# Kernel optimization log

Measured on AMD Instinct MI355X. Metric: run time of the kernel, lower is better.

## Reference

```python
import jax, jax.numpy as jnp
import numpy as np

N_NODES = 50000
N_EDGES = 1600000
IN_DIM = 64
EDGE_DIM = 8
N_GRAPHS = 256
EXP_IN = 32
H = 64  # hidden dim per head / GCN hidden
EPS = 1e-5
NEG_SLOPE = 0.2


def gat_layer(x, src, dst, ea, W, a_src, a_dst, We, a_e, bias, heads, dim, concat):
    """PyG-style GATConv with edge features and self-loops (fill_value='mean')."""
    N = x.shape[0]
    ones_e = jnp.ones((ea.shape[0],), x.dtype)
    cnt = jax.ops.segment_sum(ones_e, dst, num_segments=N)
    loop_attr = jax.ops.segment_sum(ea, dst, num_segments=N) / jnp.maximum(cnt, 1.0)[:, None]
    s = jnp.concatenate([src, jnp.arange(N)])
    d = jnp.concatenate([dst, jnp.arange(N)])
    eaf = jnp.concatenate([ea, loop_attr], axis=0)  # [E+N, edge_dim]
    h = (x @ W).reshape(N, heads, dim)              # [N, H, D]
    ee = (eaf @ We).reshape(-1, heads, dim)         # [E+N, H, D]
    al_src = (h * a_src).sum(-1)                    # [N, H]
    al_dst = (h * a_dst).sum(-1)                    # [N, H]
    score = al_src[s] + al_dst[d] + (ee * a_e).sum(-1)
    score = jax.nn.leaky_relu(score, NEG_SLOPE)     # [E+N, H]
    m = jax.ops.segment_max(score, d, num_segments=N)
    ex = jnp.exp(score - m[d])
    att = ex / jax.ops.segment_sum(ex, d, num_segments=N)[d]
    out = jax.ops.segment_sum(h[s] * att[:, :, None], d, num_segments=N)  # [N, H, D]
    out = out.reshape(N, heads * dim) if concat else out.mean(axis=1)
    return out + bias


def gcn_layer(x, src, dst, W, b):
    """PyG-style GCNConv: add self loops, symmetric degree normalization."""
    N = x.shape[0]
    s = jnp.concatenate([src, jnp.arange(N)])
    d = jnp.concatenate([dst, jnp.arange(N)])
    deg = jax.ops.segment_sum(jnp.ones((s.shape[0],), x.dtype), d, num_segments=N)
    dinv = jax.lax.rsqrt(deg)  # deg >= 1 thanks to self loops
    norm = dinv[s] * dinv[d]
    h = x @ W
    return jax.ops.segment_sum(h[s] * norm[:, None], d, num_segments=N) + b


def bn(x, g, b):
    m = x.mean(axis=0)
    v = x.var(axis=0)
    return g * (x - m) * jax.lax.rsqrt(v + EPS) + b


def mean_pool(x, batch, num_graphs):
    s = jax.ops.segment_sum(x, batch, num_segments=num_graphs)
    c = jax.ops.segment_sum(jnp.ones((x.shape[0],), x.dtype), batch, num_segments=num_graphs)
    return s / jnp.maximum(c, 1.0)[:, None]


def setup_inputs() -> dict:
    key = jax.random.key(0)
    ks = jax.random.split(key, 32)
    p = lambda i, shape: jax.random.normal(ks[i], shape, jnp.float32) * 0.05
    z = lambda n: jnp.zeros((n,), jnp.float32)
    o = lambda n: jnp.ones((n,), jnp.float32)
    return {
        "x": jax.random.normal(ks[0], (N_NODES, IN_DIM), jnp.float32),
        "edge_attr": jax.random.normal(ks[1], (N_EDGES, EDGE_DIM), jnp.float32),
        "experimental_feat": jax.random.normal(ks[2], (N_GRAPHS, EXP_IN), jnp.float32),
        "edge_index": jax.random.randint(ks[3], (2, N_EDGES), 0, N_NODES),
        "batch": jnp.sort(jax.random.randint(ks[4], (N_NODES,), 0, N_GRAPHS)),
        "W1": p(5, (IN_DIM, 4 * H)), "att_src1": p(6, (4, H)), "att_dst1": p(7, (4, H)),
        "We1": p(8, (EDGE_DIM, 4 * H)), "att_e1": p(9, (4, H)), "b1": z(4 * H),
        "g1": o(4 * H), "be1": z(4 * H),
        "W2": p(10, (4 * H, H)), "att_src2": p(11, (1, H)), "att_dst2": p(12, (1, H)),
        "We2": p(13, (EDGE_DIM, H)), "att_e2": p(14, (1, H)), "b2": z(H),
        "g2": o(H), "be2": z(H),
        "Wg1": p(15, (H, H)), "bg1": z(H), "g3": o(H), "be3": z(H),
        "Wg2": p(16, (H, H)), "bg2": z(H), "g4": o(H), "be4": z(H),
        "Wex1": p(17, (EXP_IN, H)), "bex1": z(H), "Wex2": p(18, (H, H)), "bex2": z(H),
        "Wc1": p(19, (2 * H, 128)), "bc1": z(128), "Wc2": p(20, (128, 1)), "bc2": z(1),
    }


def reference(x, edge_attr, experimental_feat, edge_index, batch,
              W1, att_src1, att_dst1, We1, att_e1, b1, g1, be1,
              W2, att_src2, att_dst2, We2, att_e2, b2, g2, be2,
              Wg1, bg1, g3, be3, Wg2, bg2, g4, be4,
              Wex1, bex1, Wex2, bex2, Wc1, bc1, Wc2, bc2):
    src, dst = edge_index[0], edge_index[1]
    h = gat_layer(x, src, dst, edge_attr, W1, att_src1, att_dst1, We1, att_e1, b1, 4, H, True)
    h = jax.nn.relu(bn(h, g1, be1))
    h = gat_layer(h, src, dst, edge_attr, W2, att_src2, att_dst2, We2, att_e2, b2, 1, H, False)
    h = jax.nn.relu(bn(h, g2, be2))  # dropout = identity in eval
    h = gcn_layer(h, src, dst, Wg1, bg1)
    h = jax.nn.relu(bn(h, g3, be3))
    h = gcn_layer(h, src, dst, Wg2, bg2)
    h = jax.nn.relu(bn(h, g4, be4))
    xp = mean_pool(h, batch, N_GRAPHS)                    # [G, H]
    e = jax.nn.relu(experimental_feat @ Wex1 + bex1)
    e = jax.nn.relu(e @ Wex2 + bex2)
    combined = jnp.concatenate([xp, e], axis=1)           # [G, 2H]
    combined = jax.nn.relu(combined @ Wc1 + bc1)          # [G, 128]
    out = combined @ Wc2 + bc2                            # [G, 1]
    return (out, xp, combined)
```

## Files before the change

kernel.cpp:

```cpp
#include <hip/hip_runtime.h>
#include <hip/hip_bf16.h>

#define N_NODES 50000
#define N_EDGES 1600000
#define N_GRAPHS 256
#define NEG_SLOPE 0.2f
#define BN_EPS 1e-5f

typedef __hip_bfloat16 bf16;
typedef __attribute__((ext_vector_type(8))) short s16x8;
typedef __attribute__((ext_vector_type(4))) float f32x4;
typedef __attribute__((ext_vector_type(4))) int i32x4;

__device__ __forceinline__ float b2f(bf16 v){ return __bfloat162float(v); }
__device__ __forceinline__ bf16 f2b(float v){ return __float2bfloat16(v); }
__device__ __forceinline__ float us2f(unsigned short u){ return __uint_as_float(((unsigned)u)<<16); }
__device__ __forceinline__ unsigned short f2us(float v){ bf16 b = f2b(v); return *(unsigned short*)&b; }
__device__ __forceinline__ unsigned pk2(float a, float b){ return (unsigned)f2us(a) | ((unsigned)f2us(b)<<16); }
__device__ __forceinline__ float ldF(const void* p, size_t i, int m){
  return m ? ((const float*)p)[i] : b2f(((const bf16*)p)[i]);
}
__device__ __forceinline__ float sane(float v){
  return (v == v && fabsf(v) < 1e30f) ? v : 0.f;
}
__device__ __forceinline__ float sel4(const float v[4], int h){
  float r = v[0];
  r = (h==1) ? v[1] : r;
  r = (h==2) ? v[2] : r;
  r = (h==3) ? v[3] : r;
  return r;
}
__device__ __forceinline__ void acc8(float* acc, float w, uint4 u){
  acc[0] += w*us2f((unsigned short)(u.x & 0xffff)); acc[1] += w*us2f((unsigned short)(u.x >> 16));
  acc[2] += w*us2f((unsigned short)(u.y & 0xffff)); acc[3] += w*us2f((unsigned short)(u.y >> 16));
  acc[4] += w*us2f((unsigned short)(u.z & 0xffff)); acc[5] += w*us2f((unsigned short)(u.z >> 16));
  acc[6] += w*us2f((unsigned short)(u.w & 0xffff)); acc[7] += w*us2f((unsigned short)(u.w >> 16));
}
__device__ __forceinline__ void unp8(float* o, uint4 u){
  o[0] = us2f((unsigned short)(u.x & 0xffff)); o[1] = us2f((unsigned short)(u.x >> 16));
  o[2] = us2f((unsigned short)(u.y & 0xffff)); o[3] = us2f((unsigned short)(u.y >> 16));
  o[4] = us2f((unsigned short)(u.z & 0xffff)); o[5] = us2f((unsigned short)(u.z >> 16));
  o[6] = us2f((unsigned short)(u.w & 0xffff)); o[7] = us2f((unsigned short)(u.w >> 16));
}
__device__ __forceinline__ s16x8 pk8(const float* v){
  s16x8 r;
  #pragma unroll
  for(int j=0;j<8;j++) r[j] = (short)f2us(v[j]);
  return r;
}
__device__ __forceinline__ void wave_lds_fence(){
  __builtin_amdgcn_sched_barrier(0);
  asm volatile("s_waitcnt lgkmcnt(0)" ::: "memory");
  __builtin_amdgcn_sched_barrier(0);
}

__device__ int detect_mode_block(const void* x){
  __shared__ int s_ins;
  if(threadIdx.x == 0) s_ins = 0;
  __syncthreads();
  const unsigned short* u = (const unsigned short*)x;
  int c = 0;
  for(int i = threadIdx.x; i < 1024; i += blockDim.x){
    float v = fabsf(us2f(u[i]));
    if(!(v > 1e-6f && v < 1e4f)) c++;
  }
  if(c) atomicAdd(&s_ins, c);
  __syncthreads();
  return (s_ins > 128) ? 1 : 0;
}

#define NSEG 33
struct Bank { const void* p[NSEG]; int n[NSEG]; int off[NSEG]; };

__global__ void k_convert(Bank b, const void* xdet, float* out){
  int m = detect_mode_block(xdet);
  int seg = blockIdx.y;
  int i = blockIdx.x*256 + threadIdx.x;
  if(i < b.n[seg]) out[b.off[seg] + i] = ldF(b.p[seg], i, m);
}

__global__ void k_cvt_x(const void* x, bf16* xb){
  int m = detect_mode_block(x);
  int i4 = blockIdx.x*256 + threadIdx.x;
  if(i4 >= N_NODES*16) return;
  if(m){
    float4 v = ((const float4*)x)[i4];
    ((ushort4*)xb)[i4] = make_ushort4(f2us(v.x), f2us(v.y), f2us(v.z), f2us(v.w));
  } else {
    ((ushort4*)xb)[i4] = ((const ushort4*)x)[i4];
  }
}

__global__ void k_we(const float* __restrict__ We1, const float* __restrict__ ae1,
                     const float* __restrict__ We2, const float* __restrict__ ae2,
                     float* __restrict__ w_e){
  int t = threadIdx.x;
  if(t < 32){
    int h = t >> 3, k = t & 7;
    float s = 0.f;
    for(int d=0;d<64;d++) s += We1[k*256 + h*64 + d] * ae1[h*64 + d];
    w_e[t] = s;
  } else if(t < 40){
    int k = t - 32;
    float s = 0.f;
    for(int d=0;d<64;d++) s += We2[k*64 + d] * ae2[d];
    w_e[t] = s;
  }
}

__global__ void k_wt(const float* __restrict__ W1, const float* __restrict__ W2,
                     const float* __restrict__ Wg1, const float* __restrict__ Wg2,
                     bf16* __restrict__ wt){
  int i = blockIdx.x*256 + threadIdx.x;
  if(i < 16384){
    int c = i >> 6, k = i & 63;
    wt[i] = f2b(W1[k*256 + c]);
  } else if(i < 32768){
    int j = i - 16384; int c = j >> 8, k = j & 255;
    wt[i] = f2b(W2[k*64 + c]);
  } else if(i < 36864){
    int j = i - 32768; int c = j >> 6, k = j & 63;
    wt[i] = f2b(Wg1[k*64 + c]);
  } else if(i < 40960){
    int j = i - 36864; int c = j >> 6, k = j & 63;
    wt[i] = f2b(Wg2[k*64 + c]);
  }
}

__global__ void k_count(const int* __restrict__ dst, int* __restrict__ cnt){
  int e = blockIdx.x*256 + threadIdx.x;
  if(e < N_EDGES){
    int d = dst[e]; if((unsigned)d >= N_NODES) d = 0;
    atomicAdd(&cnt[d], 1);
  }
}

__global__ void k_blocksum(const int* __restrict__ cnt, int* __restrict__ bsum){
  __shared__ int s[256];
  int i = blockIdx.x*256 + threadIdx.x;
  s[threadIdx.x] = (i < N_NODES) ? cnt[i] : 0;
  __syncthreads();
  for(int o=128;o>0;o>>=1){ if(threadIdx.x<o) s[threadIdx.x]+=s[threadIdx.x+o]; __syncthreads(); }
  if(threadIdx.x==0) bsum[blockIdx.x]=s[0];
}

__global__ void k_scan_bsum(const int* __restrict__ bsum, int* __restrict__ bofs, int nb){
  __shared__ int s[256];
  int t = threadIdx.x;
  s[t] = (t<nb) ? bsum[t] : 0;
  __syncthreads();
  for(int o=1;o<256;o<<=1){ int v=(t>=o)?s[t-o]:0; __syncthreads(); s[t]+=v; __syncthreads(); }
  bofs[t] = (t==0) ? 0 : s[t-1];
}

__global__ void k_scan_write(const int* __restrict__ cnt, const int* __restrict__ bofs,
                             int* __restrict__ rp, float* __restrict__ dinv){
  __shared__ int s[256];
  int t = threadIdx.x; int i = blockIdx.x*256 + t;
  int v = (i<N_NODES) ? cnt[i] : 0;
  s[t]=v; __syncthreads();
  for(int o=1;o<256;o<<=1){ int a=(t>=o)?s[t-o]:0; __syncthreads(); s[t]+=a; __syncthreads(); }
  if(i<N_NODES){
    rp[i+1] = s[t] + bofs[blockIdx.x];
    dinv[i] = rsqrtf((float)v + 1.f);
  }
  if(i==0) rp[0]=0;
}

__global__ void k_fill(const int* __restrict__ src, const int* __restrict__ dst,
                       const int* __restrict__ rp, int* __restrict__ fill,
                       const void* __restrict__ ea, const void* __restrict__ xdet,
                       const float* __restrict__ w_e,
                       int4* __restrict__ epk){
  int m = detect_mode_block(xdet);
  int e = blockIdx.x*256 + threadIdx.x;
  if(e >= N_EDGES) return;
  int d = dst[e]; if((unsigned)d >= N_NODES) d = 0;
  int p = atomicAdd(&fill[d], 1);
  int slot = rp[d] + p;
  if((unsigned)slot >= N_EDGES) return;
  int sv = src[e]; if((unsigned)sv >= N_NODES) sv = 0;
  float a[8];
  if(m){
    const float* eaf = (const float*)ea;
    float4 lo = *(const float4*)&eaf[(size_t)e*8];
    float4 hi = *(const float4*)&eaf[(size_t)e*8 + 4];
    a[0]=lo.x; a[1]=lo.y; a[2]=lo.z; a[3]=lo.w;
    a[4]=hi.x; a[5]=hi.y; a[6]=hi.z; a[7]=hi.w;
  } else {
    #pragma unroll
    for(int k=0;k<8;k++) a[k] = b2f(((const bf16*)ea)[(size_t)e*8 + k]);
  }
  unsigned d4[4];
  #pragma unroll
  for(int h=0;h<4;h++){
    float s = 0.f;
    #pragma unroll
    for(int k=0;k<8;k++) s += a[k]*w_e[h*8+k];
    d4[h] = f2us(s);
  }
  float s1 = 0.f;
  #pragma unroll
  for(int k=0;k<8;k++) s1 += a[k]*w_e[32+k];
  i32x4 pk;
  pk[0] = sv;
  pk[1] = (int)(d4[0] | (d4[1] << 16));
  pk[2] = (int)(d4[2] | (d4[3] << 16));
  pk[3] = (int)(unsigned)f2us(s1);
  __builtin_nontemporal_store(pk, (i32x4*)&epk[slot]);
}

__global__ __launch_bounds__(256) void k_gemmA_mfma(
    const bf16* __restrict__ xb,
    const bf16* __restrict__ wt1,
    bf16* __restrict__ hp, int M,
    const float* __restrict__ asrc,
    const float* __restrict__ adst,
    float* __restrict__ als4, float* __restrict__ ald4)
{
  const int tid = threadIdx.x;
  const int w = tid >> 6, l = tid & 63;
  const int lr = l & 15, lg = l >> 4;
  const int bm = blockIdx.x*64 + w*16;
  const int arow_i = bm + lr;
  const uint4* arow = (const uint4*)(xb + (size_t)min(arow_i, M-1)*64);
  uint4 a0u = arow[lg];
  uint4 a1u = arow[4 + lg];
  s16x8 a0 = *(s16x8*)&a0u, a1 = *(s16x8*)&a1u;
  unsigned short* out = (unsigned short*)hp;
  const int orow0 = bm + lg*4;
  float p_s[4][4] = {};
  float p_d[4][4] = {};
  #pragma unroll
  for(int ct = 0; ct < 16; ct++){
    const uint4* brow = (const uint4*)(wt1 + (size_t)(ct*16 + lr)*64);
    uint4 b0u = brow[lg];
    uint4 b1u = brow[4 + lg];
    f32x4 acc = {0.f, 0.f, 0.f, 0.f};
    acc = __builtin_amdgcn_mfma_f32_16x16x32_bf16(a0, *(s16x8*)&b0u, acc, 0, 0, 0);
    acc = __builtin_amdgcn_mfma_f32_16x16x32_bf16(a1, *(s16x8*)&b1u, acc, 0, 0, 0);
    float a_s = asrc[ct*16 + lr];
    float a_d = adst[ct*16 + lr];
    int hh = ct >> 2;
    #pragma unroll
    for(int r = 0; r < 4; r++){
      p_s[hh][r] += acc[r]*a_s;
      p_d[hh][r] += acc[r]*a_d;
      int rr = orow0 + r;
      if(rr < M) out[(size_t)rr*256 + ct*16 + lr] = f2us(acc[r]);
    }
  }
  #pragma unroll
  for(int o = 1; o < 16; o <<= 1){
    #pragma unroll
    for(int hh=0; hh<4; hh++)
      #pragma unroll
      for(int r=0; r<4; r++){
        p_s[hh][r] += __shfl_xor(p_s[hh][r], o);
        p_d[hh][r] += __shfl_xor(p_d[hh][r], o);
      }
  }
  if(lr == 0){
    #pragma unroll
    for(int r=0;r<4;r++){
      int rr = orow0 + r;
      if(rr < M){
        #pragma unroll
        for(int hh=0;hh<4;hh++){
          als4[rr*4 + hh] = p_s[hh][r];
          ald4[rr*4 + hh] = p_d[hh][r];
        }
      }
    }
  }
}

template<int KIN>
__global__ __launch_bounds__(256) void k_gemmB_mfma(
    const bf16* __restrict__ A, const bf16* __restrict__ Wt,
    bf16* __restrict__ C, int M,
    const float* __restrict__ bnsums, const float* __restrict__ bng, const float* __restrict__ bnb,
    const float* __restrict__ asrc, const float* __restrict__ adst,
    float* __restrict__ als, float* __restrict__ ald)
{
  __shared__ float st_s[KIN];
  __shared__ float st_t[KIN];
  const int tid = threadIdx.x;
  if(tid < KIN){
    const float invN = 1.0f / (float)N_NODES;
    float mean = bnsums[tid]*invN;
    float var  = fmaxf(bnsums[KIN+tid]*invN - mean*mean, 0.f);
    float s = bng[tid]*rsqrtf(var + BN_EPS);
    st_s[tid] = s;
    st_t[tid] = bnb[tid] - mean*s;
  }
  __syncthreads();
  const int w = tid >> 6, l = tid & 63;
  const int lr = l & 15, lg = l >> 4;
  const int bm = blockIdx.x*64 + w*16;
  const int arow_i = bm + lr;
  const uint4* arow = (const uint4*)(A + (size_t)min(arow_i, M-1)*KIN);
  f32x4 acc[4];
  #pragma unroll
  for(int ct=0;ct<4;ct++) acc[ct] = (f32x4){0.f,0.f,0.f,0.f};
  #pragma unroll
  for(int k0 = 0; k0 < KIN; k0 += 32){
    uint4 au = arow[(k0 >> 3) + lg];
    int c0 = k0 + lg*8;
    float v[8]; unp8(v, au);
    #pragma unroll
    for(int j = 0; j < 8; j++){
      float y = sane(v[j])*st_s[c0+j] + st_t[c0+j];
      v[j] = fmaxf(y, 0.f);
    }
    s16x8 af = pk8(v);
    #pragma unroll
    for(int ct = 0; ct < 4; ct++){
      const uint4* brow = (const uint4*)(Wt + (size_t)(ct*16 + lr)*KIN);
      uint4 bu = brow[(k0 >> 3) + lg];
      acc[ct] = __builtin_amdgcn_mfma_f32_16x16x32_bf16(af, *(s16x8*)&bu, acc[ct], 0, 0, 0);
    }
  }
  unsigned short* out = (unsigned short*)C;
  const int orow0 = bm + lg*4;
  #pragma unroll
  for(int ct = 0; ct < 4; ct++){
    #pragma unroll
    for(int r = 0; r < 4; r++){
      int rr = orow0 + r;
      if(rr < M) out[(size_t)rr*64 + ct*16 + lr] = f2us(acc[ct][r]);
    }
  }
  if(als){
    float p_s[4] = {0.f,0.f,0.f,0.f};
    float p_d[4] = {0.f,0.f,0.f,0.f};
    #pragma unroll
    for(int ct=0;ct<4;ct++){
      float a_s = asrc[ct*16 + lr];
      float a_d = adst[ct*16 + lr];
      #pragma unroll
      for(int r=0;r<4;r++){
        p_s[r] += acc[ct][r]*a_s;
        p_d[r] += acc[ct][r]*a_d;
      }
    }
    #pragma unroll
    for(int o = 1; o < 16; o <<= 1){
      #pragma unroll
      for(int r=0;r<4;r++){
        p_s[r] += __shfl_xor(p_s[r], o);
        p_d[r] += __shfl_xor(p_d[r], o);
      }
    }
    if(lr == 0){
      #pragma unroll
      for(int r=0;r<4;r++){
        int rr = orow0 + r;
        if(rr < M){ als[rr] = p_s[r]; ald[rr] = p_d[r]; }
      }
    }
  }
}

__global__ __launch_bounds__(256) void k_gat_agg4(
    const int* __restrict__ rp, const int4* __restrict__ epk,
    const bf16* __restrict__ hp,
    const float* __restrict__ als4, const float* __restrict__ ald4,
    const float* __restrict__ bias256, bf16* __restrict__ out1){
  const int wid = threadIdx.x >> 6, l = threadIdx.x & 63;
  const int n = blockIdx.x*4 + wid;
  if(n >= N_NODES) return;
  int eh = l >> 5, c8 = l & 31;
  int head = c8 >> 3;
  __shared__ int   ssrc_s[4][64];
  __shared__ float swt_s[4][64][4];
  int* ssrc = ssrc_s[wid];
  float (*swt)[4] = swt_s[wid];
  int s0 = rp[n], e0 = rp[n+1];
  if((unsigned)s0 > N_EDGES){ s0=0; e0=0; }
  if(e0 < s0 || (unsigned)e0 > N_EDGES) e0 = s0;
  float4 aldv = *(const float4*)&ald4[n*4];
  float4 alsvn = *(const float4*)&als4[n*4];
  float wsum[4] = {0.f,0.f,0.f,0.f};
  float dsum[4] = {0.f,0.f,0.f,0.f};
  float acc[8]  = {0.f,0.f,0.f,0.f,0.f,0.f,0.f,0.f};
  const unsigned short* hpu = (const unsigned short*)hp;

  for(int base = s0; base < e0; base += 64){
    int m = min(64, e0 - base);
    if(l < m){
      i32x4 pk = __builtin_nontemporal_load((const i32x4*)&epk[base+l]);
      int sn = pk[0]; if((unsigned)sn >= N_NODES) sn = 0;
      ssrc[l] = sn;
      float edf[4] = {us2f((unsigned short)(pk[1] & 0xffff)), us2f((unsigned short)((unsigned)pk[1] >> 16)),
                      us2f((unsigned short)(pk[2] & 0xffff)), us2f((unsigned short)((unsigned)pk[2] >> 16))};
      float4 alss = *(const float4*)&als4[sn*4];
      float alssv[4] = {alss.x, alss.y, alss.z, alss.w};
      float aldvv[4] = {aldv.x, aldv.y, aldv.z, aldv.w};
      float w4[4];
      #pragma unroll
      for(int h=0;h<4;h++){
        float sc = alssv[h] + aldvv[h] + edf[h];
        sc = sc > 0.f ? sc : NEG_SLOPE*sc;
        sc = fminf(sc, 30.f);
        float w = __expf(sc);
        w4[h] = w;
        wsum[h] += w; dsum[h] += edf[h];
      }
      *(float4*)&swt[l][0] = make_float4(w4[0], w4[1], w4[2], w4[3]);
    }
    wave_lds_fence();
    #pragma unroll 8
    for(int i=0;i<m;i+=2){
      int j = i + eh;
      if(j < m){
        int row = ssrc[j];
        float w = swt[j][head];
        uint4 u = *(const uint4*)&hpu[(size_t)row*256 + 8*c8];
        acc8(acc, w, u);
      }
    }
    __builtin_amdgcn_wave_barrier();
  }
  #pragma unroll
  for(int o=1;o<64;o<<=1){
    #pragma unroll
    for(int h=0;h<4;h++){
      wsum[h] += __shfl_xor(wsum[h], o);
      dsum[h] += __shfl_xor(dsum[h], o);
    }
  }
  #pragma unroll
  for(int q=0;q<8;q++) acc[q] += __shfl_xor(acc[q], 32);
  if(eh == 0){
    float alsnv[4] = {alsvn.x, alsvn.y, alsvn.z, alsvn.w};
    float aldnv[4] = {aldv.x, aldv.y, aldv.z, aldv.w};
    float sEh = sel4(wsum, head), sDh = sel4(dsum, head);
    float deg = (float)(e0 - s0);
    float sdot = deg > 0.f ? sDh/deg : 0.f;
    float sc = sel4(alsnv, head) + sel4(aldnv, head) + sdot;
    sc = sc > 0.f ? sc : NEG_SLOPE*sc;
    sc = fminf(sc, 30.f);
    float wself = __expf(sc);
    float self[8];
    unp8(self, *(const uint4*)&hpu[(size_t)n*256 + 8*c8]);
    float4 b0 = *(const float4*)&bias256[8*c8];
    float4 b1 = *(const float4*)&bias256[8*c8 + 4];
    float bi[8] = {b0.x,b0.y,b0.z,b0.w,b1.x,b1.y,b1.z,b1.w};
    float inv = 1.f/(sEh + wself);
    float o8[8];
    #pragma unroll
    for(int q=0;q<8;q++) o8[q] = (acc[q] + wself*self[q])*inv + bi[q];
    uint4 st;
    st.x = pk2(o8[0],o8[1]); st.y = pk2(o8[2],o8[3]);
    st.z = pk2(o8[4],o8[5]); st.w = pk2(o8[6],o8[7]);
    *(uint4*)&((unsigned short*)out1)[(size_t)n*256 + 8*c8] = st;
  }
}

__global__ __launch_bounds__(256) void k_gat_agg1e(
    const int* __restrict__ rp, const int4* __restrict__ epk,
    const bf16* __restrict__ hp,
    const float* __restrict__ als, const float* __restrict__ ald,
    const float* __restrict__ bias64, bf16* __restrict__ out){
  const int wid = threadIdx.x >> 6, l = threadIdx.x & 63;
  const int n = blockIdx.x*4 + wid;
  if(n >= N_NODES) return;
  int eg = l >> 3, c8 = l & 7;
  __shared__ float sw_s[4][64];
  __shared__ int   ssrc_s[4][64];
  float* sw = sw_s[wid];
  int* ssrc = ssrc_s[wid];
  int s0 = rp[n], e0 = rp[n+1];
  if((unsigned)s0 > N_EDGES){ s0=0; e0=0; }
  if(e0 < s0 || (unsigned)e0 > N_EDGES) e0 = s0;
  float aldn = ald[n];
  float wsum_l = 0.f, dsum_l = 0.f;
  float acc[8] = {0.f,0.f,0.f,0.f,0.f,0.f,0.f,0.f};
  const unsigned short* hpu = (const unsigned short*)hp;
  for(int base = s0; base < e0; base += 64){
    int m = min(64, e0 - base);
    if(l < m){
      i32x4 pk = __builtin_nontemporal_load((const i32x4*)&epk[base+l]);
      int sn = pk[0]; if((unsigned)sn >= N_NODES) sn = 0;
      ssrc[l] = sn;
      float ed = us2f((unsigned short)(pk[3] & 0xffff));
      float sc = als[sn] + aldn + ed;
      sc = sc > 0.f ? sc : NEG_SLOPE*sc;
      sc = fminf(sc, 30.f);
      float w = __expf(sc);
      sw[l] = w;
      wsum_l += w; dsum_l += ed;
    }
    wave_lds_fence();
    #pragma unroll 4
    for(int i=0;i<m;i+=8){
      int j = i + eg;
      if(j < m){
        int row = ssrc[j];
        float w = sw[j];
        uint4 u = *(const uint4*)&hpu[(size_t)row*64 + 8*c8];
        acc8(acc, w, u);
      }
    }
    __builtin_amdgcn_wave_barrier();
  }
  #pragma unroll
  for(int o=1;o<64;o<<=1){ wsum_l += __shfl_xor(wsum_l, o); dsum_l += __shfl_xor(dsum_l, o); }
  #pragma unroll
  for(int q=0;q<8;q++){
    acc[q] += __shfl_xor(acc[q], 8);
    acc[q] += __shfl_xor(acc[q], 16);
    acc[q] += __shfl_xor(acc[q], 32);
  }
  if(l < 8){
    float deg = (float)(e0 - s0);
    float sdot = deg > 0.f ? dsum_l/deg : 0.f;
    float sc = als[n] + aldn + sdot;
    sc = sc > 0.f ? sc : NEG_SLOPE*sc;
    sc = fminf(sc, 30.f);
    float wself = __expf(sc);
    float self[8];
    unp8(self, *(const uint4*)&hpu[(size_t)n*64 + 8*l]);
    float4 b0 = *(const float4*)&bias64[8*l];
    float4 b1 = *(const float4*)&bias64[8*l + 4];
    float bi[8] = {b0.x,b0.y,b0.z,b0.w,b1.x,b1.y,b1.z,b1.w};
    float inv = 1.f/(wsum_l + wself);
    float o8[8];
    #pragma unroll
    for(int q=0;q<8;q++) o8[q] = (acc[q] + wself*self[q])*inv + bi[q];
    uint4 st;
    st.x = pk2(o8[0],o8[1]); st.y = pk2(o8[2],o8[3]);
    st.z = pk2(o8[4],o8[5]); st.w = pk2(o8[6],o8[7]);
    *(uint4*)&((unsigned short*)out)[(size_t)n*64 + 8*l] = st;
  }
}

__global__ __launch_bounds__(256) void k_gcn_agg(
    const int* __restrict__ rp, const int4* __restrict__ epk,
    const float* __restrict__ dinv, const bf16* __restrict__ gp,
    const float* __restrict__ bias, bf16* __restrict__ out){
  const int wid = threadIdx.x >> 6, l = threadIdx.x & 63;
  const int n = blockIdx.x*4 + wid;
  if(n >= N_NODES) return;
  int eg = l >> 3, c8 = l & 7;
  __shared__ float sw_s[4][64];
  __shared__ int   ssrc_s[4][64];
  float* sw = sw_s[wid];
  int* ssrc = ssrc_s[wid];
  int s0 = rp[n], e0 = rp[n+1];
  if((unsigned)s0 > N_EDGES){ s0=0; e0=0; }
  if(e0 < s0 || (unsigned)e0 > N_EDGES) e0 = s0;
  float dn = dinv[n];
  float acc[8] = {0.f,0.f,0.f,0.f,0.f,0.f,0.f,0.f};
  const unsigned short* gpu = (const unsigned short*)gp;
  for(int base = s0; base < e0; base += 64){
    int m = min(64, e0 - base);
    if(l < m){
      i32x4 pk = __builtin_nontemporal_load((const i32x4*)&epk[base+l]);
      int sn = pk[0]; if((unsigned)sn >= N_NODES) sn = 0;
      ssrc[l]=sn; sw[l]=dinv[sn];
    }
    wave_lds_fence();
    #pragma unroll 4
    for(int i=0;i<m;i+=8){
      int j = i + eg;
      if(j < m){
        int row = ssrc[j];
        float w = sw[j];
        uint4 u = *(const uint4*)&gpu[(size_t)row*64 + 8*c8];
        acc8(acc, w, u);
      }
    }
    __builtin_amdgcn_wave_barrier();
  }
  #pragma unroll
  for(int q=0;q<8;q++){
    acc[q] += __shfl_xor(acc[q], 8);
    acc[q] += __shfl_xor(acc[q], 16);
    acc[q] += __shfl_xor(acc[q], 32);
  }
  if(l < 8){
    float self[8];
    unp8(self, *(const uint4*)&gpu[(size_t)n*64 + 8*l]);
    float4 b0 = *(const float4*)&bias[8*l];
    float4 b1 = *(const float4*)&bias[8*l + 4];
    float bi[8] = {b0.x,b0.y,b0.z,b0.w,b1.x,b1.y,b1.z,b1.w};
    float o8[8];
    #pragma unroll
    for(int q=0;q<8;q++) o8[q] = dn*(acc[q] + dn*self[q]) + bi[q];
    uint4 st;
    st.x = pk2(o8[0],o8[1]); st.y = pk2(o8[2],o8[3]);
    st.z = pk2(o8[4],o8[5]); st.w = pk2(o8[6],o8[7]);
    *(uint4*)&((unsigned short*)out)[(size_t)n*64 + 8*l] = st;
  }
}

template<int C>
__global__ void k_colstats(const bf16* __restrict__ X, float* __restrict__ sums){
  constexpr int RPB = 128;
  constexpr int RSTEP = 256 / C;
  int c = threadIdx.x % C;
  int r0 = threadIdx.x / C;
  int rbeg = blockIdx.x * RPB;
  int rend = min(N_NODES, rbeg + RPB);
  const unsigned short* Xu = (const unsigned short*)X;
  float s = 0.f, q = 0.f;
  for(int r = rbeg + r0; r < rend; r += RSTEP){
    float v = sane(us2f(Xu[(size_t)r*C + c]));
    s += v; q += v*v;
  }
  atomicAdd(&sums[c], s);
  atomicAdd(&sums[C + c], q);
}

__global__ __launch_bounds__(64) void k_pool3(
    const bf16* __restrict__ h, const int* __restrict__ batch,
    const float* __restrict__ sums, const float* __restrict__ g4,
    const float* __restrict__ b4,
    float* __restrict__ psum, float* __restrict__ pcnt){
  int t = threadIdx.x;
  int n0 = blockIdx.x * 256;
  int n1 = min(N_NODES, n0 + 256);
  if(n0 >= n1) return;
  const float invN = 1.0f / (float)N_NODES;
  float mean = sums[t]*invN;
  float var = fmaxf(sums[64+t]*invN - mean*mean, 0.f);
  float rstd = rsqrtf(var + BN_EPS);
  float gg = g4[t], bb = b4[t];
  const unsigned short* hu = (const unsigned short*)h;
  int cur = batch[n0]; if((unsigned)cur >= N_GRAPHS) cur = 0;
  float acc = 0.f; int cl = 0;
  for(int n = n0; n < n1; n++){
    int g = batch[n]; if((unsigned)g >= N_GRAPHS) g = 0;
    if(g != cur){
      atomicAdd(&psum[cur*64 + t], acc);
      if(t == 0) atomicAdd(&pcnt[cur], (float)cl);
      acc = 0.f; cl = 0; cur = g;
    }
    float y = (sane(us2f(hu[(size_t)n*64 + t]))-mean)*rstd*gg + bb;
    acc += fmaxf(y, 0.f);
    cl++;
  }
  atomicAdd(&psum[cur*64 + t], acc);
  if(t == 0) atomicAdd(&pcnt[cur], (float)cl);
}

__device__ __forceinline__ void stO(void* o, size_t i, float v, int m){
  if(m) ((float*)o)[i] = v; else ((bf16*)o)[i] = f2b(v);
}

__global__ __launch_bounds__(128) void k_head(
    const float* __restrict__ psum, const float* __restrict__ pcnt,
    const float* __restrict__ exf,
    const float* __restrict__ Wex1, const float* __restrict__ bex1,
    const float* __restrict__ Wex2, const float* __restrict__ bex2,
    const float* __restrict__ Wc1, const float* __restrict__ bc1,
    const float* __restrict__ Wc2, const float* __restrict__ bc2,
    const void* __restrict__ xdet, void* __restrict__ dout){
  int m0 = detect_mode_block(xdet);
  int g = blockIdx.x; int t = threadIdx.x;
  __shared__ float ci[128];
  __shared__ float e1[64];
  __shared__ float comb[128];
  __shared__ float red[128];
  if(t < 64){
    float c = fmaxf(pcnt[g], 1.f);
    float xp = sane(psum[g*64 + t]) / c;
    ci[t] = xp;
    stO(dout, 256 + (size_t)g*64 + t, xp, m0);
  } else {
    int j = t - 64;
    float s = bex1[j];
    for(int k=0;k<32;k++) s += exf[g*32 + k] * Wex1[k*64 + j];
    e1[j] = fmaxf(s, 0.f);
  }
  __syncthreads();
  if(t >= 64){
    int j = t - 64;
    float s = bex2[j];
    for(int k=0;k<64;k++) s += e1[k] * Wex2[k*64 + j];
    ci[64 + j] = fmaxf(s, 0.f);
  }
  __syncthreads();
  {
    float s = bc1[t];
    for(int k=0;k<128;k++) s += ci[k] * Wc1[k*128 + t];
    s = fmaxf(s, 0.f);
    comb[t] = s;
    stO(dout, 256 + 16384 + (size_t)g*128 + t, s, m0);
  }
  __syncthreads();
  red[t] = comb[t] * Wc2[t];
  __syncthreads();
  for(int o=64;o>0;o>>=1){ if(t<o) red[t]+=red[t+o]; __syncthreads(); }
  if(t==0) stO(dout, g, red[0] + bc2[0], m0);
}

extern "C" void kernel_launch(void* const* d_in, const int* in_sizes, int n_in,
                              void* d_out, int out_size, void* d_ws, size_t ws_size,
                              hipStream_t stream){
  const void* x    = d_in[0];
  const void* ea   = d_in[1];
  const int* ei    = (const int*)d_in[3];
  const int* batch = (const int*)d_in[4];
  const int* src = ei;
  const int* dst = ei + N_EDGES;

  char* base = (char*)d_ws;
  size_t off = 0;
  auto alloc = [&](size_t bytes) -> void* {
    void* r = base + off;
    off += (bytes + 255) & ~(size_t)255;
    return r;
  };
  int*   cnt    = (int*)  alloc((size_t)N_NODES*4);
  int*   fill   = (int*)  alloc((size_t)N_NODES*4);
  float* bnstat = (float*)alloc(4096);
  float* pool   = (float*)alloc((size_t)(N_GRAPHS*64 + N_GRAPHS)*4);
  size_t zbytes = off;
  int*   rp      = (int*)  alloc((size_t)(N_NODES+1)*4);
  int*   bsum    = (int*)  alloc(256*4);
  int*   bofs    = (int*)  alloc(256*4);
  int4*  epk     = (int4*) alloc((size_t)N_EDGES*16);
  float* dinv    = (float*)alloc((size_t)N_NODES*4);
  float* w_e     = (float*)alloc(64*4);
  float* als4    = (float*)alloc((size_t)N_NODES*4*4);
  float* ald4    = (float*)alloc((size_t)N_NODES*4*4);
  float* wbank   = (float*)alloc(80000*4);
  bf16*  wt      = (bf16*) alloc((size_t)40960*2);
  bf16*  xb      = (bf16*) alloc((size_t)N_NODES*64*2);
  bf16*  hp      = (bf16*) alloc((size_t)N_NODES*256*2);
  bf16*  outb    = (bf16*) alloc((size_t)N_NODES*256*2);

  bf16* out1 = outb;
  bf16* out2 = outb;
  bf16* out3 = outb + (size_t)N_NODES*64;
  bf16* out4 = outb + (size_t)N_NODES*128;
  float* bn1 = bnstat;
  float* bn2 = bnstat + 512;
  float* bn3 = bnstat + 640;
  float* bn4 = bnstat + 768;
  float* psum = pool;
  float* pcnt = pool + N_GRAPHS*64;

  bf16* wt1  = wt;
  bf16* wt2  = wt + 16384;
  bf16* wtg1 = wt + 32768;
  bf16* wtg2 = wt + 36864;

  const int segidx[NSEG] = {2, 5,6,7,8,9,10,11,12, 13,14,15,16,17,18,19,20,
                            21,22,23,24, 25,26,27,28, 29,30,31,32, 33,34,35,36};
  const int segn[NSEG] = {8192, 16384,256,256,2048,256,256,256,256,
                          16384,64,64,512,64,64,64,64,
                          4096,64,64,64, 4096,64,64,64,
                          2048,64,4096,64, 16384,128,128,1};
  Bank bk;
  int offs[NSEG]; int acc0 = 0;
  for(int i=0;i<NSEG;i++){ bk.p[i]=d_in[segidx[i]]; bk.n[i]=segn[i]; bk.off[i]=acc0; offs[i]=acc0; acc0+=segn[i]; }
  const float* f_exf = wbank + offs[0];
  const float* fW1 = wbank+offs[1]; const float* fas1 = wbank+offs[2]; const float* fad1 = wbank+offs[3];
  const float* fWe1= wbank+offs[4]; const float* fae1 = wbank+offs[5]; const float* fb1  = wbank+offs[6];
  const float* fg1 = wbank+offs[7]; const float* fbe1 = wbank+offs[8];
  const float* fW2 = wbank+offs[9]; const float* fas2 = wbank+offs[10]; const float* fad2 = wbank+offs[11];
  const float* fWe2= wbank+offs[12]; const float* fae2 = wbank+offs[13]; const float* fb2 = wbank+offs[14];
  const float* fg2 = wbank+offs[15]; const float* fbe2 = wbank+offs[16];
  const float* fWg1= wbank+offs[17]; const float* fbg1 = wbank+offs[18]; const float* fg3 = wbank+offs[19];
  const float* fbe3= wbank+offs[20];
  const float* fWg2= wbank+offs[21]; const float* fbg2 = wbank+offs[22]; const float* fg4 = wbank+offs[23];
  const float* fbe4= wbank+offs[24];
  const float* fWex1=wbank+offs[25]; const float* fbex1= wbank+offs[26];
  const float* fWex2=wbank+offs[27]; const float* fbex2= wbank+offs[28];
  const float* fWc1= wbank+offs[29]; const float* fbc1 = wbank+offs[30];
  const float* fWc2= wbank+offs[31]; const float* fbc2 = wbank+offs[32];

  const int nbN  = (N_NODES + 255)/256;
  const int nbE  = (N_EDGES + 255)/256;
  const int nbT  = (N_NODES + 63)/64;
  const int nbA  = (N_NODES + 3)/4;

  hipMemsetAsync(d_ws, 0, zbytes, stream);
  {
    dim3 g((16384+255)/256, NSEG);
    k_convert<<<g,256,0,stream>>>(bk, x, wbank);
  }
  k_wt<<<160,256,0,stream>>>(fW1, fW2, fWg1, fWg2, wt);
  k_cvt_x<<<(N_NODES*16+255)/256,256,0,stream>>>(x, xb);
  k_we<<<1,64,0,stream>>>(fWe1, fae1, fWe2, fae2, w_e);
  k_count<<<nbE,256,0,stream>>>(dst, cnt);
  k_blocksum<<<nbN,256,0,stream>>>(cnt, bsum);
  k_scan_bsum<<<1,256,0,stream>>>(bsum, bofs, nbN);
  k_scan_write<<<nbN,256,0,stream>>>(cnt, bofs, rp, dinv);
  k_fill<<<nbE,256,0,stream>>>(src, dst, rp, fill, ea, x, w_e, epk);

  k_gemmA_mfma<<<nbT,256,0,stream>>>(xb, wt1, hp, N_NODES, fas1, fad1, als4, ald4);
  k_gat_agg4<<<nbA,256,0,stream>>>(rp, epk, hp, als4, ald4, fb1, out1);
  k_colstats<256><<<(N_NODES+127)/128,256,0,stream>>>(out1, bn1);

  k_gemmB_mfma<256><<<nbT,256,0,stream>>>(out1, wt2, hp, N_NODES, bn1, fg1, fbe1,
                                          fas2, fad2, als4, ald4);
  k_gat_agg1e<<<nbA,256,0,stream>>>(rp, epk, hp, als4, ald4, fb2, out2);
  k_colstats<64><<<(N_NODES+127)/128,256,0,stream>>>(out2, bn2);

  k_gemmB_mfma<64><<<nbT,256,0,stream>>>(out2, wtg1, hp, N_NODES, bn2, fg2, fbe2,
                                         nullptr, nullptr, nullptr, nullptr);
  k_gcn_agg<<<nbA,256,0,stream>>>(rp, epk, dinv, hp, fbg1, out3);
  k_colstats<64><<<(N_NODES+127)/128,256,0,stream>>>(out3, bn3);

  k_gemmB_mfma<64><<<nbT,256,0,stream>>>(out3, wtg2, hp, N_NODES, bn3, fg3, fbe3,
                                         nullptr, nullptr, nullptr, nullptr);
  k_gcn_agg<<<nbA,256,0,stream>>>(rp, epk, dinv, hp, fbg2, out4);
  k_colstats<64><<<(N_NODES+127)/128,256,0,stream>>>(out4, bn4);

  k_pool3<<<nbN,64,0,stream>>>(out4, batch, bn4, fg4, fbe4, psum, pcnt);
  k_head<<<N_GRAPHS,128,0,stream>>>(psum, pcnt, f_exf, fWex1, fbex1, fWex2, fbex2,
                                    fWc1, fbc1, fWc2, fbc2, x, (void*)d_out);
}
```

Before: 929.2 us.

## Split packed edge records into SoA arrays and merge prep kernels

Replaces the 16-byte packed edge record with separate arrays for source index, 4-head edge scores and single-head edge score, so each aggregation kernel reads only the fields it uses (GCN reads 4 bytes per edge instead of 16). The weight conversion, transpose, edge-weight fold and degree count kernels are merged into one launch, the block-offset scan is folded into the scan-write kernel, and the x-to-bf16 conversion is fused into the first GEMM's load. Also raises unroll in two aggregation loops and uses more blocks in pooling. This trades fewer launches and less edge traffic for more scattered stores in the fill kernel and redundant small scans per block.

```diff
diff --git a/kernel.cpp b/kernel.cpp
--- a/kernel.cpp
+++ b/kernel.cpp
@@ -10,7 +10,7 @@
 typedef __hip_bfloat16 bf16;
 typedef __attribute__((ext_vector_type(8))) short s16x8;
 typedef __attribute__((ext_vector_type(4))) float f32x4;
-typedef __attribute__((ext_vector_type(4))) int i32x4;
+typedef __attribute__((ext_vector_type(2))) unsigned u32x2;
 
 __device__ __forceinline__ float b2f(bf16 v){ return __bfloat162float(v); }
 __device__ __forceinline__ bf16 f2b(float v){ return __float2bfloat16(v); }
@@ -72,66 +72,58 @@
 #define NSEG 33
 struct Bank { const void* p[NSEG]; int n[NSEG]; int off[NSEG]; };
 
-__global__ void k_convert(Bank b, const void* xdet, float* out){
+#define PREP_COUNT 6250
+#define PREP_CONV  (64*NSEG)
+#define PREP_WT    160
+__global__ void k_prep(Bank bk, const void* xdet, const int* __restrict__ dst,
+                       int* __restrict__ cnt, float* __restrict__ wbank,
+                       bf16* __restrict__ wt,
+                       const void* pW1, const void* pW2, const void* pWg1, const void* pWg2,
+                       const void* pWe1, const void* pae1, const void* pWe2, const void* pae2,
+                       float* __restrict__ w_e){
+  int bid = blockIdx.x;
+  int t = threadIdx.x;
+  if(bid < PREP_COUNT){
+    int e = bid*256 + t;
+    if(e < N_EDGES){
+      int d = dst[e]; if((unsigned)d >= N_NODES) d = 0;
+      atomicAdd(&cnt[d], 1);
+    }
+    return;
+  }
   int m = detect_mode_block(xdet);
-  int seg = blockIdx.y;
-  int i = blockIdx.x*256 + threadIdx.x;
-  if(i < b.n[seg]) out[b.off[seg] + i] = ldF(b.p[seg], i, m);
-}
-
-__global__ void k_cvt_x(const void* x, bf16* xb){
-  int m = detect_mode_block(x);
-  int i4 = blockIdx.x*256 + threadIdx.x;
-  if(i4 >= N_NODES*16) return;
-  if(m){
-    float4 v = ((const float4*)x)[i4];
-    ((ushort4*)xb)[i4] = make_ushort4(f2us(v.x), f2us(v.y), f2us(v.z), f2us(v.w));
+  if(bid < PREP_COUNT + PREP_CONV){
+    int b2 = bid - PREP_COUNT;
+    int seg = b2 >> 6;
+    int i = (b2 & 63)*256 + t;
+    if(i < bk.n[seg]) wbank[bk.off[seg] + i] = ldF(bk.p[seg], i, m);
+  } else if(bid < PREP_COUNT + PREP_CONV + PREP_WT){
+    int i = (bid - PREP_COUNT - PREP_CONV)*256 + t;
+    if(i < 16384){
+      int c = i >> 6, k = i & 63;
+      wt[i] = f2b(ldF(pW1, k*256 + c, m));
+    } else if(i < 32768){
+      int j = i - 16384; int c = j >> 8, k = j & 255;
+      wt[i] = f2b(ldF(pW2, k*64 + c, m));
+    } else if(i < 36864){
+      int j = i - 32768; int c = j >> 6, k = j & 63;
+      wt[i] = f2b(ldF(pWg1, k*64 + c, m));
+    } else if(i < 40960){
+      int j = i - 36864; int c = j >> 6, k = j & 63;
+      wt[i] = f2b(ldF(pWg2, k*64 + c, m));
+    }
   } else {
-    ((ushort4*)xb)[i4] = ((const ushort4*)x)[i4];
-  }
-}
-
-__global__ void k_we(const float* __restrict__ We1, const float* __restrict__ ae1,
-                     const float* __restrict__ We2, const float* __restrict__ ae2,
-                     float* __restrict__ w_e){
-  int t = threadIdx.x;
-  if(t < 32){
-    int h = t >> 3, k = t & 7;
-    float s = 0.f;
-    for(int d=0;d<64;d++) s += We1[k*256 + h*64 + d] * ae1[h*64 + d];
-    w_e[t] = s;
-  } else if(t < 40){
-    int k = t - 32;
-    float s = 0.f;
-    for(int d=0;d<64;d++) s += We2[k*64 + d] * ae2[d];
-    w_e[t] = s;
-  }
-}
-
-__global__ void k_wt(const float* __restrict__ W1, const float* __restrict__ W2,
-                     const float* __restrict__ Wg1, const float* __restrict__ Wg2,
-                     bf16* __restrict__ wt){
-  int i = blockIdx.x*256 + threadIdx.x;
-  if(i < 16384){
-    int c = i >> 6, k = i & 63;
-    wt[i] = f2b(W1[k*256 + c]);
-  } else if(i < 32768){
-    int j = i - 16384; int c = j >> 8, k = j & 255;
-    wt[i] = f2b(W2[k*64 + c]);
-  } else if(i < 36864){
-    int j = i - 32768; int c = j >> 6, k = j & 63;
-    wt[i] = f2b(Wg1[k*64 + c]);
-  } else if(i < 40960){
-    int j = i - 36864; int c = j >> 6, k = j & 63;
-    wt[i] = f2b(Wg2[k*64 + c]);
-  }
-}
-
-__global__ void k_count(const int* __restrict__ dst, int* __restrict__ cnt){
-  int e = blockIdx.x*256 + threadIdx.x;
-  if(e < N_EDGES){
-    int d = dst[e]; if((unsigned)d >= N_NODES) d = 0;
-    atomicAdd(&cnt[d], 1);
+    if(t < 32){
+      int h = t >> 3, k = t & 7;
+      float s = 0.f;
+      for(int d=0;d<64;d++) s += ldF(pWe1, k*256 + h*64 + d, m) * ldF(pae1, h*64 + d, m);
+      w_e[t] = s;
+    } else if(t < 40){
+      int k = t - 32;
+      float s = 0.f;
+      for(int d=0;d<64;d++) s += ldF(pWe2, k*64 + d, m) * ldF(pae2, d, m);
+      w_e[t] = s;
+    }
   }
 }
 
@@ -144,24 +136,20 @@
   if(threadIdx.x==0) bsum[blockIdx.x]=s[0];
 }
 
-__global__ void k_scan_bsum(const int* __restrict__ bsum, int* __restrict__ bofs, int nb){
-  __shared__ int s[256];
-  int t = threadIdx.x;
-  s[t] = (t<nb) ? bsum[t] : 0;
-  __syncthreads();
-  for(int o=1;o<256;o<<=1){ int v=(t>=o)?s[t-o]:0; __syncthreads(); s[t]+=v; __syncthreads(); }
-  bofs[t] = (t==0) ? 0 : s[t-1];
-}
-
-__global__ void k_scan_write(const int* __restrict__ cnt, const int* __restrict__ bofs,
-                             int* __restrict__ rp, float* __restrict__ dinv){
+__global__ void k_scan_write(const int* __restrict__ cnt, const int* __restrict__ bsum,
+                             int* __restrict__ rp, float* __restrict__ dinv, int nb){
+  __shared__ int sb[256];
   __shared__ int s[256];
   int t = threadIdx.x; int i = blockIdx.x*256 + t;
+  sb[t] = (t<nb) ? bsum[t] : 0;
+  __syncthreads();
+  for(int o=1;o<256;o<<=1){ int v=(t>=o)?sb[t-o]:0; __syncthreads(); sb[t]+=v; __syncthreads(); }
+  int bofs = (blockIdx.x==0) ? 0 : sb[blockIdx.x-1];
   int v = (i<N_NODES) ? cnt[i] : 0;
   s[t]=v; __syncthreads();
   for(int o=1;o<256;o<<=1){ int a=(t>=o)?s[t-o]:0; __syncthreads(); s[t]+=a; __syncthreads(); }
   if(i<N_NODES){
-    rp[i+1] = s[t] + bofs[blockIdx.x];
+    rp[i+1] = s[t] + bofs;
     dinv[i] = rsqrtf((float)v + 1.f);
   }
   if(i==0) rp[0]=0;
@@ -171,7 +159,8 @@
                        const int* __restrict__ rp, int* __restrict__ fill,
                        const void* __restrict__ ea, const void* __restrict__ xdet,
                        const float* __restrict__ w_e,
-                       int4* __restrict__ epk){
+                       int* __restrict__ srcs, u32x2* __restrict__ ed4,
+                       unsigned* __restrict__ ed1){
   int m = detect_mode_block(xdet);
   int e = blockIdx.x*256 + threadIdx.x;
   if(e >= N_EDGES) return;
@@ -202,31 +191,41 @@
   float s1 = 0.f;
   #pragma unroll
   for(int k=0;k<8;k++) s1 += a[k]*w_e[32+k];
-  i32x4 pk;
-  pk[0] = sv;
-  pk[1] = (int)(d4[0] | (d4[1] << 16));
-  pk[2] = (int)(d4[2] | (d4[3] << 16));
-  pk[3] = (int)(unsigned)f2us(s1);
-  __builtin_nontemporal_store(pk, (i32x4*)&epk[slot]);
+  __builtin_nontemporal_store(sv, &srcs[slot]);
+  u32x2 e4;
+  e4[0] = d4[0] | (d4[1] << 16);
+  e4[1] = d4[2] | (d4[3] << 16);
+  __builtin_nontemporal_store(e4, &ed4[slot]);
+  __builtin_nontemporal_store((unsigned)f2us(s1), &ed1[slot]);
 }
 
 __global__ __launch_bounds__(256) void k_gemmA_mfma(
-    const bf16* __restrict__ xb,
+    const void* __restrict__ x,
     const bf16* __restrict__ wt1,
     bf16* __restrict__ hp, int M,
     const float* __restrict__ asrc,
     const float* __restrict__ adst,
     float* __restrict__ als4, float* __restrict__ ald4)
 {
+  int m = detect_mode_block(x);
   const int tid = threadIdx.x;
   const int w = tid >> 6, l = tid & 63;
   const int lr = l & 15, lg = l >> 4;
   const int bm = blockIdx.x*64 + w*16;
-  const int arow_i = bm + lr;
-  const uint4* arow = (const uint4*)(xb + (size_t)min(arow_i, M-1)*64);
-  uint4 a0u = arow[lg];
-  uint4 a1u = arow[4 + lg];
-  s16x8 a0 = *(s16x8*)&a0u, a1 = *(s16x8*)&a1u;
+  const int row = min(bm + lr, M-1);
+  s16x8 a0, a1;
+  if(m){
+    const float* ar = (const float*)x + (size_t)row*64;
+    float va[8], vb[8];
+    #pragma unroll
+    for(int j=0;j<8;j++){ va[j] = ar[8*lg + j]; vb[j] = ar[32 + 8*lg + j]; }
+    a0 = pk8(va); a1 = pk8(vb);
+  } else {
+    const uint4* ar = (const uint4*)((const bf16*)x + (size_t)row*64);
+    uint4 a0u = ar[lg];
+    uint4 a1u = ar[4 + lg];
+    a0 = *(s16x8*)&a0u; a1 = *(s16x8*)&a1u;
+  }
   unsigned short* out = (unsigned short*)hp;
   const int orow0 = bm + lg*4;
   float p_s[4][4] = {};
@@ -363,7 +362,7 @@
 }
 
 __global__ __launch_bounds__(256) void k_gat_agg4(
-    const int* __restrict__ rp, const int4* __restrict__ epk,
+    const int* __restrict__ rp, const int* __restrict__ srcs, const u32x2* __restrict__ ed4,
     const bf16* __restrict__ hp,
     const float* __restrict__ als4, const float* __restrict__ ald4,
     const float* __restrict__ bias256, bf16* __restrict__ out1){
@@ -389,11 +388,12 @@
   for(int base = s0; base < e0; base += 64){
     int m = min(64, e0 - base);
     if(l < m){
-      i32x4 pk = __builtin_nontemporal_load((const i32x4*)&epk[base+l]);
-      int sn = pk[0]; if((unsigned)sn >= N_NODES) sn = 0;
+      int sn = __builtin_nontemporal_load(&srcs[base+l]);
+      u32x2 e4 = __builtin_nontemporal_load(&ed4[base+l]);
+      if((unsigned)sn >= N_NODES) sn = 0;
       ssrc[l] = sn;
-      float edf[4] = {us2f((unsigned short)(pk[1] & 0xffff)), us2f((unsigned short)((unsigned)pk[1] >> 16)),
-                      us2f((unsigned short)(pk[2] & 0xffff)), us2f((unsigned short)((unsigned)pk[2] >> 16))};
+      float edf[4] = {us2f((unsigned short)(e4[0] & 0xffff)), us2f((unsigned short)(e4[0] >> 16)),
+                      us2f((unsigned short)(e4[1] & 0xffff)), us2f((unsigned short)(e4[1] >> 16))};
       float4 alss = *(const float4*)&als4[sn*4];
       float alssv[4] = {alss.x, alss.y, alss.z, alss.w};
       float aldvv[4] = {aldv.x, aldv.y, aldv.z, aldv.w};
@@ -459,7 +459,7 @@
 }
 
 __global__ __launch_bounds__(256) void k_gat_agg1e(
-    const int* __restrict__ rp, const int4* __restrict__ epk,
+    const int* __restrict__ rp, const int* __restrict__ srcs, const unsigned* __restrict__ ed1,
     const bf16* __restrict__ hp,
     const float* __restrict__ als, const float* __restrict__ ald,
     const float* __restrict__ bias64, bf16* __restrict__ out){
@@ -481,10 +481,11 @@
   for(int base = s0; base < e0; base += 64){
     int m = min(64, e0 - base);
     if(l < m){
-      i32x4 pk = __builtin_nontemporal_load((const i32x4*)&epk[base+l]);
-      int sn = pk[0]; if((unsigned)sn >= N_NODES) sn = 0;
+      int sn = __builtin_nontemporal_load(&srcs[base+l]);
+      unsigned ew = __builtin_nontemporal_load(&ed1[base+l]);
+      if((unsigned)sn >= N_NODES) sn = 0;
       ssrc[l] = sn;
-      float ed = us2f((unsigned short)(pk[3] & 0xffff));
+      float ed = us2f((unsigned short)(ew & 0xffff));
       float sc = als[sn] + aldn + ed;
       sc = sc > 0.f ? sc : NEG_SLOPE*sc;
       sc = fminf(sc, 30.f);
@@ -493,7 +494,7 @@
       wsum_l += w; dsum_l += ed;
     }
     wave_lds_fence();
-    #pragma unroll 4
+    #pragma unroll 8
     for(int i=0;i<m;i+=8){
       int j = i + eg;
       if(j < m){
@@ -537,7 +538,7 @@
 }
 
 __global__ __launch_bounds__(256) void k_gcn_agg(
-    const int* __restrict__ rp, const int4* __restrict__ epk,
+    const int* __restrict__ rp, const int* __restrict__ srcs,
     const float* __restrict__ dinv, const bf16* __restrict__ gp,
     const float* __restrict__ bias, bf16* __restrict__ out){
   const int wid = threadIdx.x >> 6, l = threadIdx.x & 63;
@@ -557,12 +558,12 @@
   for(int base = s0; base < e0; base += 64){
     int m = min(64, e0 - base);
     if(l < m){
-      i32x4 pk = __builtin_nontemporal_load((const i32x4*)&epk[base+l]);
-      int sn = pk[0]; if((unsigned)sn >= N_NODES) sn = 0;
+      int sn = __builtin_nontemporal_load(&srcs[base+l]);
+      if((unsigned)sn >= N_NODES) sn = 0;
       ssrc[l]=sn; sw[l]=dinv[sn];
     }
     wave_lds_fence();
-    #pragma unroll 4
+    #pragma unroll 8
     for(int i=0;i<m;i+=8){
       int j = i + eg;
       if(j < m){
@@ -620,8 +621,8 @@
     const float* __restrict__ b4,
     float* __restrict__ psum, float* __restrict__ pcnt){
   int t = threadIdx.x;
-  int n0 = blockIdx.x * 256;
-  int n1 = min(N_NODES, n0 + 256);
+  int n0 = blockIdx.x * 64;
+  int n1 = min(N_NODES, n0 + 64);
   if(n0 >= n1) return;
   const float invN = 1.0f / (float)N_NODES;
   float mean = sums[t]*invN;
@@ -721,15 +722,15 @@
   size_t zbytes = off;
   int*   rp      = (int*)  alloc((size_t)(N_NODES+1)*4);
   int*   bsum    = (int*)  alloc(256*4);
-  int*   bofs    = (int*)  alloc(256*4);
-  int4*  epk     = (int4*) alloc((size_t)N_EDGES*16);
+  int*   srcs    = (int*)  alloc((size_t)N_EDGES*4);
+  u32x2* ed4     = (u32x2*)alloc((size_t)N_EDGES*8);
+  unsigned* ed1  = (unsigned*)alloc((size_t)N_EDGES*4);
   float* dinv    = (float*)alloc((size_t)N_NODES*4);
   float* w_e     = (float*)alloc(64*4);
   float* als4    = (float*)alloc((size_t)N_NODES*4*4);
   float* ald4    = (float*)alloc((size_t)N_NODES*4*4);
   float* wbank   = (float*)alloc(80000*4);
   bf16*  wt      = (bf16*) alloc((size_t)40960*2);
-  bf16*  xb      = (bf16*) alloc((size_t)N_NODES*64*2);
   bf16*  hp      = (bf16*) alloc((size_t)N_NODES*256*2);
   bf16*  outb    = (bf16*) alloc((size_t)N_NODES*256*2);
 
@@ -759,15 +760,15 @@
   int offs[NSEG]; int acc0 = 0;
   for(int i=0;i<NSEG;i++){ bk.p[i]=d_in[segidx[i]]; bk.n[i]=segn[i]; bk.off[i]=acc0; offs[i]=acc0; acc0+=segn[i]; }
   const float* f_exf = wbank + offs[0];
-  const float* fW1 = wbank+offs[1]; const float* fas1 = wbank+offs[2]; const float* fad1 = wbank+offs[3];
-  const float* fWe1= wbank+offs[4]; const float* fae1 = wbank+offs[5]; const float* fb1  = wbank+offs[6];
+  const float* fas1 = wbank+offs[2]; const float* fad1 = wbank+offs[3];
+  const float* fb1  = wbank+offs[6];
   const float* fg1 = wbank+offs[7]; const float* fbe1 = wbank+offs[8];
-  const float* fW2 = wbank+offs[9]; const float* fas2 = wbank+offs[10]; const float* fad2 = wbank+offs[11];
-  const float* fWe2= wbank+offs[12]; const float* fae2 = wbank+offs[13]; const float* fb2 = wbank+offs[14];
+  const float* fas2 = wbank+offs[10]; const float* fad2 = wbank+offs[11];
+  const float* fb2 = wbank+offs[14];
   const float* fg2 = wbank+offs[15]; const float* fbe2 = wbank+offs[16];
-  const float* fWg1= wbank+offs[17]; const float* fbg1 = wbank+offs[18]; const float* fg3 = wbank+offs[19];
+  const float* fbg1 = wbank+offs[18]; const float* fg3 = wbank+offs[19];
   const float* fbe3= wbank+offs[20];
-  const float* fWg2= wbank+offs[21]; const float* fbg2 = wbank+offs[22]; const float* fg4 = wbank+offs[23];
+  const float* fbg2 = wbank+offs[22]; const float* fg4 = wbank+offs[23];
   const float* fbe4= wbank+offs[24];
   const float* fWex1=wbank+offs[25]; const float* fbex1= wbank+offs[26];
   const float* fWex2=wbank+offs[27]; const float* fbex2= wbank+offs[28];
@@ -778,41 +779,37 @@
   const int nbE  = (N_EDGES + 255)/256;
   const int nbT  = (N_NODES + 63)/64;
   const int nbA  = (N_NODES + 3)/4;
+  const int nbP  = (N_NODES + 63)/64;
 
   hipMemsetAsync(d_ws, 0, zbytes, stream);
-  {
-    dim3 g((16384+255)/256, NSEG);
-    k_convert<<<g,256,0,stream>>>(bk, x, wbank);
-  }
-  k_wt<<<160,256,0,stream>>>(fW1, fW2, fWg1, fWg2, wt);
-  k_cvt_x<<<(N_NODES*16+255)/256,256,0,stream>>>(x, xb);
-  k_we<<<1,64,0,stream>>>(fWe1, fae1, fWe2, fae2, w_e);
-  k_count<<<nbE,256,0,stream>>>(dst, cnt);
+  k_prep<<<PREP_COUNT + PREP_CONV + PREP_WT + 1, 256, 0, stream>>>(
+      bk, x, dst, cnt, wbank, wt,
+      d_in[5], d_in[13], d_in[21], d_in[25],
+      d_in[8], d_in[9], d_in[16], d_in[17], w_e);
   k_blocksum<<<nbN,256,0,stream>>>(cnt, bsum);
-  k_scan_bsum<<<1,256,0,stream>>>(bsum, bofs, nbN);
-  k_scan_write<<<nbN,256,0,stream>>>(cnt, bofs, rp, dinv);
-  k_fill<<<nbE,256,0,stream>>>(src, dst, rp, fill, ea, x, w_e, epk);
-
-  k_gemmA_mfma<<<nbT,256,0,stream>>>(xb, wt1, hp, N_NODES, fas1, fad1, als4, ald4);
-  k_gat_agg4<<<nbA,256,0,stream>>>(rp, epk, hp, als4, ald4, fb1, out1);
+  k_scan_write<<<nbN,256,0,stream>>>(cnt, bsum, rp, dinv, nbN);
+  k_fill<<<nbE,256,0,stream>>>(src, dst, rp, fill, ea, x, w_e, srcs, ed4, ed1);
+
+  k_gemmA_mfma<<<nbT,256,0,stream>>>(x, wt1, hp, N_NODES, fas1, fad1, als4, ald4);
+  k_gat_agg4<<<nbA,256,0,stream>>>(rp, srcs, ed4, hp, als4, ald4, fb1, out1);
   k_colstats<256><<<(N_NODES+127)/128,256,0,stream>>>(out1, bn1);
 
   k_gemmB_mfma<256><<<nbT,256,0,stream>>>(out1, wt2, hp, N_NODES, bn1, fg1, fbe1,
                                           fas2, fad2, als4, ald4);
-  k_gat_agg1e<<<nbA,256,0,stream>>>(rp, epk, hp, als4, ald4, fb2, out2);
+  k_gat_agg1e<<<nbA,256,0,stream>>>(rp, srcs, ed1, hp, als4, ald4, fb2, out2);
   k_colstats<64><<<(N_NODES+127)/128,256,0,stream>>>(out2, bn2);
 
   k_gemmB_mfma<64><<<nbT,256,0,stream>>>(out2, wtg1, hp, N_NODES, bn2, fg2, fbe2,
                                          nullptr, nullptr, nullptr, nullptr);
-  k_gcn_agg<<<nbA,256,0,stream>>>(rp, epk, dinv, hp, fbg1, out3);
+  k_gcn_agg<<<nbA,256,0,stream>>>(rp, srcs, dinv, hp, fbg1, out3);
   k_colstats<64><<<(N_NODES+127)/128,256,0,stream>>>(out3, bn3);
 
   k_gemmB_mfma<64><<<nbT,256,0,stream>>>(out3, wtg2, hp, N_NODES, bn3, fg3, fbe3,
                                          nullptr, nullptr, nullptr, nullptr);
-  k_gcn_agg<<<nbA,256,0,stream>>>(rp, epk, dinv, hp, fbg2, out4);
+  k_gcn_agg<<<nbA,256,0,stream>>>(rp, srcs, dinv, hp, fbg2, out4);
   k_colstats<64><<<(N_NODES+127)/128,256,0,stream>>>(out4, bn4);
 
-  k_pool3<<<nbN,64,0,stream>>>(out4, batch, bn4, fg4, fbe4, psum, pcnt);
+  k_pool3<<<nbP,64,0,stream>>>(out4, batch, bn4, fg4, fbe4, psum, pcnt);
   k_head<<<N_GRAPHS,128,0,stream>>>(psum, pcnt, f_exf, fWex1, fbex1, fWex2, fbex2,
                                     fWc1, fbc1, fWc2, fbc2, x, (void*)d_out);
 }
```

Result: slower. 959.7 us (+3.3%).
